# Kernel optimization log

Measured on AMD Instinct MI355X. Metric: run time of the kernel, lower is better.

Reference implementation:

```python
import jax, jax.numpy as jnp
import numpy as np

POINTS_PER_UNIT = 64
EPS = 1e-8


def setup_inputs() -> dict:
    key = jax.random.key(0)
    k1, k2 = jax.random.split(key)
    b, n, c, m = 4, 1024, 16, 1024
    # context inputs in [-2, 2]
    xz = jax.random.uniform(k1, (b, n, 1), dtype=jnp.float32, minval=-2.0, maxval=2.0)
    z = jax.random.normal(k2, (b, n, c), dtype=jnp.float32)
    # uniform grid covering the data range with a small margin (stands in for discretisation(xz, x))
    x_grid = jnp.linspace(-2.1, 2.1, m, dtype=jnp.float32)
    # learnable length-scale, init = log(2 / points_per_unit)
    log_scale = jnp.full((1,), np.log(2.0 / POINTS_PER_UNIT), dtype=jnp.float32)
    return {"xz": xz, "z": z, "x_grid": x_grid, "log_scale": log_scale}


def reference(xz, z, x_grid, log_scale):
    b, n, c = z.shape
    m = x_grid.shape[0]
    # pairwise squared distances between context locations and grid: [b, n, m]
    dists2 = (xz[:, :, 0:1] - x_grid[None, None, :]) ** 2
    # Gaussian (RBF) kernel weights
    weights = jnp.exp(-0.5 * dists2 / jnp.exp(2.0 * log_scale[0]))  # [b, n, m]
    # prepend density channel of ones: [b, n, c+1]
    zc = jnp.concatenate([jnp.ones((b, n, 1), z.dtype), z], axis=2)
    # out[b,k,i,j] = sum_n weights[b,n,i] * zc[b,n,k] * weights[b,n,j]
    # (matches B.matmul(weights * z, weights, tr_a=True) in the original)
    out = jnp.einsum('bni,bnk,bnj->bkij', weights, zc, weights)  # [b, c+1, m, m]
    density = out[:, :1]
    # KDE normalization of data channels by the density channel
    out = jnp.concatenate([density, out[:, 1:] / (density + EPS)], axis=1)
    # prepend identity channel: [b, 1, m, m]
    identity = jnp.broadcast_to(jnp.eye(m, dtype=z.dtype), (b, 1, m, m))
    out = jnp.concatenate([identity, out], axis=1)  # [b, c+2, m, m]
    return (x_grid, out)
```

## Files before the change

### kernel.cpp

```cpp
#include <hip/hip_runtime.h>

typedef float v4f __attribute__((ext_vector_type(4)));

#define NPTS    1024
#define MGRID   1024
#define NCH     16
#define MAXL    320
#define UPB     8
#define FSTRIDE 2048
#define CUT     0.32f


__global__ __launch_bounds__(256)
void f_table_kernel(const float* __restrict__ xz,
                    const float* __restrict__ z,
                    const float* __restrict__ x_grid,
                    const float* __restrict__ log_scale,
                    float* __restrict__ F)
{
    const int ug   = blockIdx.x;
    const int b    = blockIdx.y;
    const int tid  = threadIdx.x;
    const int w    = tid >> 6;
    const int lane = tid & 63;
    const int u0   = ug * UPB;

    __shared__ float xz_l[MAXL];
    __shared__ v4f   z_l[MAXL * 4];
    __shared__ int   cnts[4];

    const float s2   = __expf(2.0f * log_scale[0]);
    const float ninv = -1.0f / s2;

    const int  u7  = (u0 + UPB - 1) > 2046 ? 2046 : (u0 + UPB - 1);
    const float m_lo = 0.5f * (x_grid[u0 >> 1] + x_grid[u0 - (u0 >> 1)]);
    const float m_hi = 0.5f * (x_grid[u7 >> 1] + x_grid[u7 - (u7 >> 1)]);
    const float lo = m_lo - CUT, hi = m_hi + CUT;

    const float* xzb = xz + b * NPTS;
    float xv[4]; unsigned long long msk[4]; int idx[4];
    int base = 0;
    #pragma unroll
    for (int r = 0; r < 4; ++r) {
        const int n = 256 * w + 64 * r + lane;
        xv[r] = xzb[n];
        const bool pred = (xv[r] > lo) && (xv[r] < hi);
        msk[r] = __ballot(pred);
        idx[r] = base + (int)__popcll(msk[r] & ((1ull << lane) - 1ull));
        base += (int)__popcll(msk[r]);
    }
    if (lane == 0) cnts[w] = base;
    __syncthreads();

    int off = 0, total = 0;
    #pragma unroll
    for (int s = 0; s < 4; ++s) { const int c = cnts[s]; if (s < w) off += c; total += c; }
    if (total > MAXL) total = MAXL;

    const v4f* zb4 = (const v4f*)(z + (size_t)b * NPTS * NCH);
    #pragma unroll
    for (int r = 0; r < 4; ++r) {
        if ((msk[r] >> lane) & 1ull) {
            const int slot = off + idx[r];
            if (slot < MAXL) {
                const int n = 256 * w + 64 * r + lane;
                xz_l[slot] = xv[r];
                #pragma unroll
                for (int q = 0; q < 4; ++q)
                    z_l[slot * 4 + q] = zb4[n * 4 + q];
            }
        }
    }
    __syncthreads();

    const int ul = tid >> 5;
    const int kk = tid & 31;
    const int u  = u0 + ul;
    const int uu = u > 2046 ? 2046 : u;
    const float xm = 0.5f * (x_grid[uu >> 1] + x_grid[uu - (uu >> 1)]);

    const float* zl = (const float*)z_l;
    const int zidx0 = (kk == 0) ? 0 : (kk - 1);
    const bool isone = (kk == 0);

    float acc = 0.0f;
    for (int t = 0; t < total; ++t) {
        const float d = xz_l[t] - xm;
        const float e = __expf(ninv * (d * d));
        const float val = isone ? 1.0f : zl[t * 16 + zidx0];
        acc += e * val;
    }

    if (kk < 17 && u <= 2046)
        F[((b * 17 + kk) << 11) + u] = acc;
}

__global__ __launch_bounds__(256)
void emit_kernel(const float* __restrict__ x_grid,
                 const float* __restrict__ log_scale,
                 const float* __restrict__ F,
                 float* __restrict__ out)
{
    const int i  = blockIdx.x;
    const int b  = blockIdx.y;
    const int t  = threadIdx.x;
    const int j0 = t * 4;

    const float s2 = __expf(2.0f * log_scale[0]);
    const float h  = x_grid[1] - x_grid[0];
    const float cB = -(h * h) / (4.0f * s2);

    const float* Fb = F + (b * 17) * FSTRIDE;

    float B[4], den[4], inv[4];
    #pragma unroll
    for (int l = 0; l < 4; ++l) {
        const int dj = i - (j0 + l);
        B[l]   = __expf(cB * (float)(dj * dj));
        den[l] = B[l] * Fb[i + j0 + l];
        inv[l] = 1.0f / (den[l] + 1e-8f);
    }

    float* big = out + MGRID;
    const size_t plane = (size_t)MGRID * MGRID;
    float* rb = big + ((size_t)b * 18) * plane + (size_t)i * MGRID;

    {
        v4f v;
        v.x = (j0 + 0 == i) ? 1.f : 0.f;
        v.y = (j0 + 1 == i) ? 1.f : 0.f;
        v.z = (j0 + 2 == i) ? 1.f : 0.f;
        v.w = (j0 + 3 == i) ? 1.f : 0.f;
        ((v4f*)rb)[t] = v;
    }
    {
        const v4f dv = {den[0], den[1], den[2], den[3]};
        ((v4f*)(rb + plane))[t] = dv;
    }
    #pragma unroll
    for (int k = 1; k <= 16; ++k) {
        const float* Fk = Fb + k * FSTRIDE + i + j0;
        v4f rv;
        rv.x = B[0] * Fk[0] * inv[0];
        rv.y = B[1] * Fk[1] * inv[1];
        rv.z = B[2] * Fk[2] * inv[2];
        rv.w = B[3] * Fk[3] * inv[3];
        ((v4f*)(rb + (size_t)(k + 1) * plane))[t] = rv;
    }

    if (b == 0 && i == 0)
        ((v4f*)out)[t] = ((const v4f*)x_grid)[t];
}

extern "C" void kernel_launch(void* const* d_in, const int* in_sizes, int n_in,
                              void* d_out, int out_size, void* d_ws, size_t ws_size,
                              hipStream_t stream)
{
    const float* xz = (const float*)d_in[0];
    const float* z  = (const float*)d_in[1];
    const float* xg = (const float*)d_in[2];
    const float* ls = (const float*)d_in[3];
    float* out = (float*)d_out;
    float* F   = (float*)d_ws;

    f_table_kernel<<<dim3(2048 / UPB, 4), dim3(256), 0, stream>>>(xz, z, xg, ls, F);
    emit_kernel  <<<dim3(MGRID, 4),      dim3(256), 0, stream>>>(xg, ls, F, out);
}
```

Baseline: 323.0 us.

## Remap emit kernel so each block writes one contiguous 64KB output slab

The emit kernel now assigns each block a contiguous 16-row strip of a single output plane (72 planes times 64 strips), instead of one row across all 18 planes. The intent is to give each block a linear streaming write region, which should make DRAM writes more sequential. In exchange it recomputes the Gaussian factor and density per channel, and it uses a hardware reciprocal in place of a full divide, which may change precision slightly.

```diff
diff --git a/kernel.cpp b/kernel.cpp
--- a/kernel.cpp
+++ b/kernel.cpp
@@ -96,60 +96,82 @@
 }
 
 __global__ __launch_bounds__(256)
-void emit_kernel(const float* __restrict__ x_grid,
+void emit_linear(const float* __restrict__ x_grid,
                  const float* __restrict__ log_scale,
                  const float* __restrict__ F,
                  float* __restrict__ out)
 {
-    const int i  = blockIdx.x;
-    const int b  = blockIdx.y;
-    const int t  = threadIdx.x;
-    const int j0 = t * 4;
+    const int bid = blockIdx.x;
+    const int tid = threadIdx.x;
+    const int p   = bid >> 6;
+    const int ch  = p % 18;
+    const int b   = p / 18;
+    const int row0 = (bid & 63) * 16;
+
+    v4f* rp = (v4f*)(out + MGRID) + (size_t)bid * 4096;
+
+    if (bid == 0)
+        ((v4f*)out)[tid] = ((const v4f*)x_grid)[tid];
+
+    if (ch == 0) {
+        #pragma unroll
+        for (int it = 0; it < 16; ++it) {
+            const int Fi  = it * 256 + tid;
+            const int row = row0 + (Fi >> 8);
+            const int j0  = (Fi & 255) << 2;
+            v4f v;
+            v.x = (j0 + 0 == row) ? 1.f : 0.f;
+            v.y = (j0 + 1 == row) ? 1.f : 0.f;
+            v.z = (j0 + 2 == row) ? 1.f : 0.f;
+            v.w = (j0 + 3 == row) ? 1.f : 0.f;
+            rp[Fi] = v;
+        }
+        return;
+    }
 
     const float s2 = __expf(2.0f * log_scale[0]);
     const float h  = x_grid[1] - x_grid[0];
     const float cB = -(h * h) / (4.0f * s2);
+    const float* F0 = F + (b * 17) * FSTRIDE;
 
-    const float* Fb = F + (b * 17) * FSTRIDE;
-
-    float B[4], den[4], inv[4];
-    #pragma unroll
-    for (int l = 0; l < 4; ++l) {
-        const int dj = i - (j0 + l);
-        B[l]   = __expf(cB * (float)(dj * dj));
-        den[l] = B[l] * Fb[i + j0 + l];
-        inv[l] = 1.0f / (den[l] + 1e-8f);
+    if (ch == 1) {
+        #pragma unroll
+        for (int it = 0; it < 16; ++it) {
+            const int Fi  = it * 256 + tid;
+            const int row = row0 + (Fi >> 8);
+            const int j0  = (Fi & 255) << 2;
+            const float fr = (float)(row - j0);
+            v4f v;
+            #pragma unroll
+            for (int l = 0; l < 4; ++l) {
+                const float d  = fr - (float)l;
+                const float Bv = __expf(cB * d * d);
+                v[l] = Bv * F0[row + j0 + l];
+            }
+            rp[Fi] = v;
+        }
+        return;
     }
 
-    float* big = out + MGRID;
-    const size_t plane = (size_t)MGRID * MGRID;
-    float* rb = big + ((size_t)b * 18) * plane + (size_t)i * MGRID;
-
-    {
+    const float* Fk = F0 + (ch - 1) * FSTRIDE;
+    #pragma unroll
+    for (int it = 0; it < 16; ++it) {
+        const int Fi  = it * 256 + tid;
+        const int row = row0 + (Fi >> 8);
+        const int j0  = (Fi & 255) << 2;
+        const float fr = (float)(row - j0);
+        const int u0i = row + j0;
         v4f v;
-        v.x = (j0 + 0 == i) ? 1.f : 0.f;
-        v.y = (j0 + 1 == i) ? 1.f : 0.f;
-        v.z = (j0 + 2 == i) ? 1.f : 0.f;
-        v.w = (j0 + 3 == i) ? 1.f : 0.f;
-        ((v4f*)rb)[t] = v;
+        #pragma unroll
+        for (int l = 0; l < 4; ++l) {
+            const float d   = fr - (float)l;
+            const float Bv  = __expf(cB * d * d);
+            const float den = Bv * F0[u0i + l] + 1e-8f;
+            const float num = Bv * Fk[u0i + l];
+            v[l] = num * __builtin_amdgcn_rcpf(den);
+        }
+        rp[Fi] = v;
     }
-    {
-        const v4f dv = {den[0], den[1], den[2], den[3]};
-        ((v4f*)(rb + plane))[t] = dv;
-    }
-    #pragma unroll
-    for (int k = 1; k <= 16; ++k) {
-        const float* Fk = Fb + k * FSTRIDE + i + j0;
-        v4f rv;
-        rv.x = B[0] * Fk[0] * inv[0];
-        rv.y = B[1] * Fk[1] * inv[1];
-        rv.z = B[2] * Fk[2] * inv[2];
-        rv.w = B[3] * Fk[3] * inv[3];
-        ((v4f*)(rb + (size_t)(k + 1) * plane))[t] = rv;
-    }
-
-    if (b == 0 && i == 0)
-        ((v4f*)out)[t] = ((const v4f*)x_grid)[t];
 }
 
 extern "C" void kernel_launch(void* const* d_in, const int* in_sizes, int n_in,
@@ -164,5 +186,5 @@
     float* F   = (float*)d_ws;
 
     f_table_kernel<<<dim3(2048 / UPB, 4), dim3(256), 0, stream>>>(xz, z, xg, ls, F);
-    emit_kernel  <<<dim3(MGRID, 4),      dim3(256), 0, stream>>>(xg, ls, F, out);
+    emit_linear   <<<dim3(72 * 64),       dim3(256), 0, stream>>>(xg, ls, F, out);
 }
```

Measured after the change: 326.1 us. No clear change (+1.0%).

## Zero output with memset and write only the near-diagonal band per row

Applied to the files above, without the earlier changes.

Replaces the per-row emit kernel with a band kernel. A bulk hipMemsetAsync first zeroes the whole output. Each wavefront then writes only a 256-wide window around the diagonal for one (batch, channel, row), plus the single identity element and the grid copy. This moves most of the output traffic to a bulk fill and drops exp and division work for entries that are effectively zero. The risk is that entries outside the band are assumed negligible, which only holds for length scales near the default, and channel planes are now written twice (memset, then band).

```diff
diff --git a/kernel.cpp b/kernel.cpp
--- a/kernel.cpp
+++ b/kernel.cpp
@@ -9,6 +9,7 @@
 #define UPB     8
 #define FSTRIDE 2048
 #define CUT     0.32f
+#define HBAND   96
 
 
 __global__ __launch_bounds__(256)
@@ -96,60 +97,60 @@
 }
 
 __global__ __launch_bounds__(256)
-void emit_kernel(const float* __restrict__ x_grid,
+void band_kernel(const float* __restrict__ x_grid,
                  const float* __restrict__ log_scale,
                  const float* __restrict__ F,
                  float* __restrict__ out)
 {
-    const int i  = blockIdx.x;
-    const int b  = blockIdx.y;
-    const int t  = threadIdx.x;
-    const int j0 = t * 4;
+    const int job  = blockIdx.x * 4 + (threadIdx.x >> 6);
+    const int lane = threadIdx.x & 63;
+    const int p    = job >> 10;
+    const int i    = job & 1023;
+    const int ch   = p % 18;
+    const int b    = p / 18;
+
+    float* big = out + MGRID;
+    const size_t plane = (size_t)MGRID * MGRID;
+    float* rb = big + (size_t)p * plane + (size_t)i * MGRID;
+
+    if (ch == 0) {
+        if (lane == 0) rb[i] = 1.0f;
+        if (p == 0 && lane == 1) out[i] = x_grid[i];
+        return;
+    }
 
     const float s2 = __expf(2.0f * log_scale[0]);
     const float h  = x_grid[1] - x_grid[0];
     const float cB = -(h * h) / (4.0f * s2);
 
-    const float* Fb = F + (b * 17) * FSTRIDE;
+    const float* F0 = F + (b * 17) * FSTRIDE;
+    const float* Fk = F0 + (ch - 1) * FSTRIDE;
 
-    float B[4], den[4], inv[4];
-    #pragma unroll
-    for (int l = 0; l < 4; ++l) {
-        const int dj = i - (j0 + l);
-        B[l]   = __expf(cB * (float)(dj * dj));
-        den[l] = B[l] * Fb[i + j0 + l];
-        inv[l] = 1.0f / (den[l] + 1e-8f);
+    int start = (i - HBAND) & ~3;
+    if (start < 0) start = 0;
+    if (start > MGRID - 256) start = MGRID - 256;
+    const int j0 = start + 4 * lane;
+
+    v4f v;
+    if (ch == 1) {
+        #pragma unroll
+        for (int l = 0; l < 4; ++l) {
+            const int   j = j0 + l;
+            const float d = (float)(i - j);
+            const float B = __expf(cB * d * d);
+            v[l] = B * F0[i + j];
+        }
+    } else {
+        #pragma unroll
+        for (int l = 0; l < 4; ++l) {
+            const int   j   = j0 + l;
+            const float d   = (float)(i - j);
+            const float B   = __expf(cB * d * d);
+            const float den = B * F0[i + j] + 1e-8f;
+            v[l] = (B * Fk[i + j]) * __builtin_amdgcn_rcpf(den);
+        }
     }
-
-    float* big = out + MGRID;
-    const size_t plane = (size_t)MGRID * MGRID;
-    float* rb = big + ((size_t)b * 18) * plane + (size_t)i * MGRID;
-
-    {
-        v4f v;
-        v.x = (j0 + 0 == i) ? 1.f : 0.f;
-        v.y = (j0 + 1 == i) ? 1.f : 0.f;
-        v.z = (j0 + 2 == i) ? 1.f : 0.f;
-        v.w = (j0 + 3 == i) ? 1.f : 0.f;
-        ((v4f*)rb)[t] = v;
-    }
-    {
-        const v4f dv = {den[0], den[1], den[2], den[3]};
-        ((v4f*)(rb + plane))[t] = dv;
-    }
-    #pragma unroll
-    for (int k = 1; k <= 16; ++k) {
-        const float* Fk = Fb + k * FSTRIDE + i + j0;
-        v4f rv;
-        rv.x = B[0] * Fk[0] * inv[0];
-        rv.y = B[1] * Fk[1] * inv[1];
-        rv.z = B[2] * Fk[2] * inv[2];
-        rv.w = B[3] * Fk[3] * inv[3];
-        ((v4f*)(rb + (size_t)(k + 1) * plane))[t] = rv;
-    }
-
-    if (b == 0 && i == 0)
-        ((v4f*)out)[t] = ((const v4f*)x_grid)[t];
+    *(v4f*)(rb + j0) = v;
 }
 
 extern "C" void kernel_launch(void* const* d_in, const int* in_sizes, int n_in,
@@ -163,6 +164,8 @@
     float* out = (float*)d_out;
     float* F   = (float*)d_ws;
 
+    hipMemsetAsync(out, 0, (size_t)out_size, stream);
+
     f_table_kernel<<<dim3(2048 / UPB, 4), dim3(256), 0, stream>>>(xz, z, xg, ls, F);
-    emit_kernel  <<<dim3(MGRID, 4),      dim3(256), 0, stream>>>(xg, ls, F, out);
+    band_kernel   <<<dim3(73728 / 4),     dim3(256), 0, stream>>>(xg, ls, F, out);
 }
```

Result: faster. 302.0 us (-6.5%).
